# Optimization experiments

Measured on AMD Instinct MI355X. Metric: run time of the kernel, lower is better.

## Reference

```python
import jax, jax.numpy as jnp
import numpy as np

N_HEAD = 16
RMS_EPS = 1.1920928955078125e-07  # torch float32 finfo eps (F.rms_norm default)


def _apply_rotary(x, cos, sin):
    # x: [B,T,H,D], cos/sin: [1,T,1,D/2]
    d = x.shape[-1] // 2
    x1, x2 = x[..., :d], x[..., d:]
    return jnp.concatenate([x1 * cos + x2 * sin, -x1 * sin + x2 * cos], axis=-1)


def _rms_norm(x):
    var = jnp.mean(jnp.square(x), axis=-1, keepdims=True)
    return x * jax.lax.rsqrt(var + RMS_EPS)


def setup_inputs() -> dict:
    key = jax.random.key(0)
    ks = jax.random.split(key, 5)
    B, T, C, H = 2, 2048, 1024, N_HEAD
    D = C // H
    x = jax.random.normal(ks[0], (B, T, C), dtype=jnp.float32)
    cos = jax.random.uniform(ks[1], (1, T, 1, D // 2), dtype=jnp.float32)
    sin = jax.random.uniform(ks[2], (1, T, 1, D // 2), dtype=jnp.float32)
    kv_w = jax.random.normal(ks[3], (C, C), dtype=jnp.float32) * (C ** -0.5)
    proj_w = jax.random.normal(ks[4], (C, C), dtype=jnp.float32) * (C ** -0.5)
    return {"x": x, "cos": cos, "sin": sin, "kv_w": kv_w, "proj_w": proj_w, "window_left": 1024}


def reference(x, cos, sin, kv_w, proj_w, window_left):
    B, T, C = x.shape
    H = N_HEAD
    D = C // H
    scale = D ** -0.5

    q = x.reshape(B, T, H, D)                       # no Q projection
    kv = (x @ kv_w.T).reshape(B, T, H, D)           # tied K=V projection

    q = _rms_norm(_apply_rotary(q, cos, sin))
    kv = _rms_norm(_apply_rotary(kv, cos, sin))

    # scores: [B,H,T,T]
    scores = jnp.einsum('bqhd,bkhd->bhqk', q, kv) * scale

    pos = jnp.arange(T)
    dist = pos[:, None] - pos[None, :]              # query_pos - key_pos
    allowed = (dist >= 0) & (dist <= window_left)   # causal + sliding window
    scores = jnp.where(allowed[None, None], scores, -jnp.inf)

    attn = jax.nn.softmax(scores, axis=-1)
    out = jnp.einsum('bhqk,bkhd->bqhd', attn, kv).reshape(B, T, C)
    return out @ proj_w.T
```

## Files before the change

kernel.cpp:

```cpp
#include <hip/hip_runtime.h>
#include <hip/hip_bf16.h>

using u16 = unsigned short;
typedef __attribute__((ext_vector_type(8))) short short8v;
typedef __attribute__((ext_vector_type(4))) float f32x4;

#define MFMA16(a, b, c) __builtin_amdgcn_mfma_f32_16x16x32_bf16((a), (b), (c), 0, 0, 0)

#define GLOAD16(g, l) __builtin_amdgcn_global_load_lds(                       \
    (const __attribute__((address_space(1))) void*)(const void*)(g),          \
    (__attribute__((address_space(3))) void*)(void*)(l), 16, 0, 0)

static __device__ __forceinline__ u16 f2bf(float x) {
  __hip_bfloat16 h = __float2bfloat16(x);
  return __builtin_bit_cast(u16, h);
}

__global__ __launch_bounds__(256) void cast3_f32_bf16(const float* __restrict__ a, u16* __restrict__ da,
                                                      const float* __restrict__ b, u16* __restrict__ db,
                                                      const float* __restrict__ c, u16* __restrict__ dc) {
  int bid = blockIdx.x;
  const float* s; u16* d; int i;
  if (bid < 4096)      { s = a; d = da; i = bid; }
  else if (bid < 5120) { s = b; d = db; i = bid - 4096; }
  else                 { s = c; d = dc; i = bid - 5120; }
  int idx = (i * 256 + threadIdx.x) * 4;
  float4 v = *reinterpret_cast<const float4*>(s + idx);
  ushort4 o;
  o.x = f2bf(v.x); o.y = f2bf(v.y); o.z = f2bf(v.z); o.w = f2bf(v.w);
  *reinterpret_cast<ushort4*>(d + idx) = o;
}

__global__ __launch_bounds__(256) void gemm_bt(const u16* __restrict__ A,
                                               const u16* __restrict__ Bt,
                                               float* __restrict__ C,
                                               int M, int N, int K) {
  __shared__ u16 As[4][64 * 32];
  __shared__ u16 Bs[4][128 * 32];
  unsigned flat = blockIdx.y * gridDim.x + blockIdx.x;
  unsigned nwg = gridDim.x * gridDim.y;
  unsigned swz = (flat & 7) * (nwg >> 3) + (flat >> 3);
  int bm = swz % gridDim.x, bn = swz / gridDim.x;
  int tid = threadIdx.x;
  int wid = tid >> 6, l = tid & 63, lr = l & 15, lg = l >> 4;
  int wr = wid >> 1, wc = wid & 1;

  int srow = l >> 2, scol = (l & 3) * 8;
  const u16* Ag  = A  + (size_t)(bm * 64 + wid * 16 + srow) * K + scol;
  const u16* Bg0 = Bt + (size_t)(bn * 128 + wid * 32 + srow) * K + scol;
  const u16* Bg1 = Bg0 + (size_t)16 * K;

  f32x4 acc[2][4];
#pragma unroll
  for (int m = 0; m < 2; m++)
#pragma unroll
    for (int n = 0; n < 4; n++) acc[m][n] = (f32x4){0.f, 0.f, 0.f, 0.f};

  const int NT = K >> 5;

#pragma unroll
  for (int t = 0; t < 2; t++) {
    GLOAD16(Ag + t * 32, &As[t][wid * 512]);
    GLOAD16(Bg0 + t * 32, &Bs[t][wid * 1024]);
    GLOAD16(Bg1 + t * 32, &Bs[t][wid * 1024 + 512]);
  }

  for (int t = 0; t < NT; t++) {
    int cur = t & 3;
    if (t + 2 < NT) {
      int nb = (t + 2) & 3;
      int ko = (t + 2) * 32;
      GLOAD16(Ag + ko, &As[nb][wid * 512]);
      GLOAD16(Bg0 + ko, &Bs[nb][wid * 1024]);
      GLOAD16(Bg1 + ko, &Bs[nb][wid * 1024 + 512]);
    }
    if (t + 2 < NT)      asm volatile("s_waitcnt vmcnt(6)" ::: "memory");
    else if (t + 1 < NT) asm volatile("s_waitcnt vmcnt(3)" ::: "memory");
    else                 asm volatile("s_waitcnt vmcnt(0)" ::: "memory");
    __builtin_amdgcn_s_barrier();

    short8v af[2], bfr[4];
#pragma unroll
    for (int m = 0; m < 2; m++)
      af[m] = *reinterpret_cast<const short8v*>(&As[cur][(wr * 32 + m * 16 + lr) * 32 + lg * 8]);
#pragma unroll
    for (int n = 0; n < 4; n++)
      bfr[n] = *reinterpret_cast<const short8v*>(&Bs[cur][(wc * 64 + n * 16 + lr) * 32 + lg * 8]);
    asm volatile("s_waitcnt lgkmcnt(0)" ::: "memory");
    __builtin_amdgcn_sched_barrier(0);
    __builtin_amdgcn_s_setprio(1);
#pragma unroll
    for (int m = 0; m < 2; m++)
#pragma unroll
      for (int n = 0; n < 4; n++) acc[m][n] = MFMA16(af[m], bfr[n], acc[m][n]);
    __builtin_amdgcn_s_setprio(0);
  }

#pragma unroll
  for (int m = 0; m < 2; m++)
#pragma unroll
    for (int n = 0; n < 4; n++)
#pragma unroll
      for (int r = 0; r < 4; r++) {
        int row = bm * 64 + wr * 32 + m * 16 + lg * 4 + r;
        int col = bn * 128 + wc * 64 + n * 16 + lr;
        C[(size_t)row * N + col] = acc[m][n][r];
      }
}

__global__ __launch_bounds__(256) void rope_rms(const float* __restrict__ src,
                                                u16* __restrict__ dst,
                                                const float* __restrict__ cosp,
                                                const float* __restrict__ sinp,
                                                float scale) {
  int R = blockIdx.x * 4 + (threadIdx.x >> 6);
  int l = threadIdx.x & 63;
  int h = R & 15;
  int bt = R >> 4;
  int t = bt & 2047, b = bt >> 11;

  float v = src[((size_t)R << 6) + l];
  float p = __shfl_xor(v, 32);
  float c = cosp[(t << 5) + (l & 31)];
  float s = sinp[(t << 5) + (l & 31)];
  float r = v * c + ((l < 32) ? p * s : -p * s);
  float sq = r * r;
  sq += __shfl_xor(sq, 32);
  sq += __shfl_xor(sq, 16);
  sq += __shfl_xor(sq, 8);
  sq += __shfl_xor(sq, 4);
  sq += __shfl_xor(sq, 2);
  sq += __shfl_xor(sq, 1);
  float inv = rsqrtf(sq * (1.0f / 64.0f) + 1.1920928955078125e-07f) * scale;
  dst[((((size_t)b * 16 + h) * 2048 + t) << 6) + l] = f2bf(r * inv);
}

__global__ __launch_bounds__(256) void rope_rms_kv(const float* __restrict__ src,
                                                   u16* __restrict__ dst,
                                                   u16* __restrict__ dstT,
                                                   const float* __restrict__ cosp,
                                                   const float* __restrict__ sinp) {
  __shared__ u16 Ld[64][72];
  int t0 = blockIdx.x << 6;
  int bh = blockIdx.y;
  int b = bh >> 4, h = bh & 15;
  int tid = threadIdx.x;
  int w = tid >> 6, l = tid & 63;

  float cl, sl;
  for (int i = 0; i < 16; i++) {
    int tt = w * 16 + i;
    int t = t0 + tt;
    float v = src[((((size_t)b * 2048 + t) * 16 + h) << 6) + l];
    float p = __shfl_xor(v, 32);
    cl = cosp[(t << 5) + (l & 31)];
    sl = sinp[(t << 5) + (l & 31)];
    float r = v * cl + ((l < 32) ? p * sl : -p * sl);
    float sq = r * r;
    sq += __shfl_xor(sq, 32);
    sq += __shfl_xor(sq, 16);
    sq += __shfl_xor(sq, 8);
    sq += __shfl_xor(sq, 4);
    sq += __shfl_xor(sq, 2);
    sq += __shfl_xor(sq, 1);
    float inv = rsqrtf(sq * (1.0f / 64.0f) + 1.1920928955078125e-07f);
    u16 val = f2bf(r * inv);
    dst[(((size_t)bh * 2048 + t) << 6) + l] = val;
    Ld[tt][l] = val;
  }
  __syncthreads();
#pragma unroll
  for (int i = 0; i < 2; i++) {
    int c = tid + i * 256, dr = c >> 3, sg = c & 7;
    short8v v;
#pragma unroll
    for (int j = 0; j < 8; j++) v[j] = (short)Ld[sg * 8 + j][dr];
    *reinterpret_cast<short8v*>(dstT + ((size_t)bh * 64 + dr) * 2048 + t0 + sg * 8) = v;
  }
}

__global__ __launch_bounds__(256) void attn_swa(const u16* __restrict__ Q,
                                                const u16* __restrict__ KV,
                                                const u16* __restrict__ KVt,
                                                u16* __restrict__ O,
                                                const int* __restrict__ winp) {
  const int T = 2048;
  int bid = blockIdx.x;
  int bh = bid & 31;
  int qi = 31 - (bid >> 5);
  int q0 = qi << 6;
  int b = bh >> 4, h = bh & 15;
  int W = *winp;
  int tid = threadIdx.x;
  int wid = tid >> 6, l = tid & 63, lr = l & 15, lg = l >> 4;

  __shared__ u16 Kl[64][72];
  __shared__ u16 Vt[64][72];
  __shared__ u16 Pl[4][16][72];

  const u16* Qb = Q + (((size_t)bh * T + q0 + wid * 16 + lr) << 6);
  short8v aq0 = *reinterpret_cast<const short8v*>(Qb + lg * 8);
  short8v aq1 = *reinterpret_cast<const short8v*>(Qb + 32 + lg * 8);

  const short one_bf = (short)0x3F80;
  short8v vones = {one_bf, one_bf, one_bf, one_bf, one_bf, one_bf, one_bf, one_bf};

  float l_run[4];
  f32x4 oacc[4];
#pragma unroll
  for (int r = 0; r < 4; r++) l_run[r] = 0.f;
#pragma unroll
  for (int dt = 0; dt < 4; dt++) oacc[dt] = (f32x4){0.f, 0.f, 0.f, 0.f};

  int lo = q0 - W;
  if (lo < 0) lo = 0;
  lo &= ~63;

  const u16* KVbh  = KV + (((size_t)bh * T) << 6);
  const u16* KVtbh = KVt + ((size_t)bh << 6) * T;
  int r8 = tid >> 3, sg = tid & 7;

  short8v vK0 = *reinterpret_cast<const short8v*>(KVbh + ((size_t)(lo + r8) << 6) + sg * 8);
  short8v vK1 = *reinterpret_cast<const short8v*>(KVbh + ((size_t)(lo + r8 + 32) << 6) + sg * 8);
  short8v vV0 = *reinterpret_cast<const short8v*>(KVtbh + (size_t)r8 * T + lo + sg * 8);
  short8v vV1 = *reinterpret_cast<const short8v*>(KVtbh + (size_t)(r8 + 32) * T + lo + sg * 8);

  for (int kt = lo; kt <= q0; kt += 64) {
    __syncthreads();
    *reinterpret_cast<short8v*>(&Kl[r8][sg * 8]) = vK0;
    *reinterpret_cast<short8v*>(&Kl[r8 + 32][sg * 8]) = vK1;
    *reinterpret_cast<short8v*>(&Vt[r8][sg * 8]) = vV0;
    *reinterpret_cast<short8v*>(&Vt[r8 + 32][sg * 8]) = vV1;
    __syncthreads();
    if (kt < q0) {
      vK0 = *reinterpret_cast<const short8v*>(KVbh + ((size_t)(kt + 64 + r8) << 6) + sg * 8);
      vK1 = *reinterpret_cast<const short8v*>(KVbh + ((size_t)(kt + 64 + r8 + 32) << 6) + sg * 8);
      vV0 = *reinterpret_cast<const short8v*>(KVtbh + (size_t)r8 * T + kt + 64 + sg * 8);
      vV1 = *reinterpret_cast<const short8v*>(KVtbh + (size_t)(r8 + 32) * T + kt + 64 + sg * 8);
    }

    f32x4 s[4];
#pragma unroll
    for (int nt = 0; nt < 4; nt++) {
      s[nt] = (f32x4){0.f, 0.f, 0.f, 0.f};
      short8v b0 = *reinterpret_cast<const short8v*>(&Kl[nt * 16 + lr][lg * 8]);
      s[nt] = MFMA16(aq0, b0, s[nt]);
      short8v b1 = *reinterpret_cast<const short8v*>(&Kl[nt * 16 + lr][32 + lg * 8]);
      s[nt] = MFMA16(aq1, b1, s[nt]);
    }

    bool edge = (kt + 63 > q0 + wid * 16) || ((q0 - kt) + wid * 16 + 15 > W);
#pragma unroll
    for (int r = 0; r < 4; r++) {
      if (edge) {
        int t = q0 + wid * 16 + lg * 4 + r;
#pragma unroll
        for (int nt = 0; nt < 4; nt++) {
          int k = kt + nt * 16 + lr;
          float val = ((k <= t) && (t - k <= W)) ? s[nt][r] : -1e30f;
          Pl[wid][lg * 4 + r][nt * 16 + lr] = f2bf(exp2f(val - 12.f));
        }
      } else {
#pragma unroll
        for (int nt = 0; nt < 4; nt++)
          Pl[wid][lg * 4 + r][nt * 16 + lr] = f2bf(exp2f(s[nt][r] - 12.f));
      }
    }

    short8v ap0 = *reinterpret_cast<const short8v*>(&Pl[wid][lr][lg * 8]);
    short8v ap1 = *reinterpret_cast<const short8v*>(&Pl[wid][lr][32 + lg * 8]);
    f32x4 psum = (f32x4){0.f, 0.f, 0.f, 0.f};
    psum = MFMA16(ap0, vones, psum);
    psum = MFMA16(ap1, vones, psum);
#pragma unroll
    for (int dt = 0; dt < 4; dt++) {
      short8v v0 = *reinterpret_cast<const short8v*>(&Vt[dt * 16 + lr][lg * 8]);
      oacc[dt] = MFMA16(ap0, v0, oacc[dt]);
      short8v v1 = *reinterpret_cast<const short8v*>(&Vt[dt * 16 + lr][32 + lg * 8]);
      oacc[dt] = MFMA16(ap1, v1, oacc[dt]);
    }
#pragma unroll
    for (int r = 0; r < 4; r++) l_run[r] += psum[r];
  }

#pragma unroll
  for (int r = 0; r < 4; r++) {
    int t = q0 + wid * 16 + lg * 4 + r;
    float inv = 1.f / l_run[r];
#pragma unroll
    for (int dt = 0; dt < 4; dt++) {
      O[(((size_t)b * T + t) << 10) + (h << 6) + dt * 16 + lr] = f2bf(oacc[dt][r] * inv);
    }
  }
}

extern "C" void kernel_launch(void* const* d_in, const int* in_sizes, int n_in,
                              void* d_out, int out_size, void* d_ws, size_t ws_size,
                              hipStream_t stream) {
  (void)in_sizes; (void)n_in; (void)out_size; (void)ws_size;
  const float* x    = (const float*)d_in[0];
  const float* cosp = (const float*)d_in[1];
  const float* sinp = (const float*)d_in[2];
  const float* kvw  = (const float*)d_in[3];
  const float* pw   = (const float*)d_in[4];
  const int*   win  = (const int*)d_in[5];

  char* w = (char*)d_ws;
  u16*   xbf   = (u16*)(w);
  u16*   kvwbf = (u16*)(w + (8u << 20));
  u16*   pwbf  = (u16*)(w + (10u << 20));
  float* kvf   = (float*)(w + (12u << 20));
  u16*   kvt   = (u16*)(w + (12u << 20));
  u16*   aout  = (u16*)(w + (20u << 20));
  u16*   kvbf  = (u16*)(w + (28u << 20));
  u16*   qbf   = xbf;
  kvt = (u16*)(w + (36u << 20));

  cast3_f32_bf16<<<6144, 256, 0, stream>>>(x, xbf, kvw, kvwbf, pw, pwbf);

  gemm_bt<<<dim3(64, 8), 256, 0, stream>>>(xbf, kvwbf, kvf, 4096, 1024, 1024);

  rope_rms<<<16384, 256, 0, stream>>>(x, qbf, cosp, sinp, 0.18033688011112042f);
  rope_rms_kv<<<dim3(32, 32), 256, 0, stream>>>(kvf, kvbf, kvt, cosp, sinp);

  attn_swa<<<1024, 256, 0, stream>>>(qbf, kvbf, kvt, aout, win);

  gemm_bt<<<dim3(64, 8), 256, 0, stream>>>(aout, pwbf, (float*)d_out, 4096, 1024, 1024);
}
```

Measured before the change: 180.8 us.

## Split-K both GEMMs into two halves and fuse x cast into rope kernel

After: 192.5 us. 1.06x slower.

```diff
diff --git a/kernel.cpp b/kernel.cpp
--- a/kernel.cpp
+++ b/kernel.cpp
@@ -16,14 +16,12 @@
   return __builtin_bit_cast(u16, h);
 }
 
-__global__ __launch_bounds__(256) void cast3_f32_bf16(const float* __restrict__ a, u16* __restrict__ da,
-                                                      const float* __restrict__ b, u16* __restrict__ db,
-                                                      const float* __restrict__ c, u16* __restrict__ dc) {
+__global__ __launch_bounds__(256) void cast2_f32_bf16(const float* __restrict__ a, u16* __restrict__ da,
+                                                      const float* __restrict__ b, u16* __restrict__ db) {
   int bid = blockIdx.x;
   const float* s; u16* d; int i;
-  if (bid < 4096)      { s = a; d = da; i = bid; }
-  else if (bid < 5120) { s = b; d = db; i = bid - 4096; }
-  else                 { s = c; d = dc; i = bid - 5120; }
+  if (bid < 1024) { s = a; d = da; i = bid; }
+  else            { s = b; d = db; i = bid - 1024; }
   int idx = (i * 256 + threadIdx.x) * 4;
   float4 v = *reinterpret_cast<const float4*>(s + idx);
   ushort4 o;
@@ -31,24 +29,36 @@
   *reinterpret_cast<ushort4*>(d + idx) = o;
 }
 
+__global__ __launch_bounds__(256) void reduce2(const float* __restrict__ p0,
+                                               const float* __restrict__ p1,
+                                               float* __restrict__ out) {
+  int i = (blockIdx.x * 256 + threadIdx.x) * 4;
+  float4 a = *reinterpret_cast<const float4*>(p0 + i);
+  float4 b = *reinterpret_cast<const float4*>(p1 + i);
+  float4 o = {a.x + b.x, a.y + b.y, a.z + b.z, a.w + b.w};
+  *reinterpret_cast<float4*>(out + i) = o;
+}
+
 __global__ __launch_bounds__(256) void gemm_bt(const u16* __restrict__ A,
                                                const u16* __restrict__ Bt,
                                                float* __restrict__ C,
-                                               int M, int N, int K) {
+                                               int M, int N, int K, int K2) {
   __shared__ u16 As[4][64 * 32];
   __shared__ u16 Bs[4][128 * 32];
   unsigned flat = blockIdx.y * gridDim.x + blockIdx.x;
   unsigned nwg = gridDim.x * gridDim.y;
   unsigned swz = (flat & 7) * (nwg >> 3) + (flat >> 3);
   int bm = swz % gridDim.x, bn = swz / gridDim.x;
+  int z = blockIdx.z;
   int tid = threadIdx.x;
   int wid = tid >> 6, l = tid & 63, lr = l & 15, lg = l >> 4;
   int wr = wid >> 1, wc = wid & 1;
 
   int srow = l >> 2, scol = (l & 3) * 8;
-  const u16* Ag  = A  + (size_t)(bm * 64 + wid * 16 + srow) * K + scol;
-  const u16* Bg0 = Bt + (size_t)(bn * 128 + wid * 32 + srow) * K + scol;
+  const u16* Ag  = A  + (size_t)(bm * 64 + wid * 16 + srow) * K + z * K2 + scol;
+  const u16* Bg0 = Bt + (size_t)(bn * 128 + wid * 32 + srow) * K + z * K2 + scol;
   const u16* Bg1 = Bg0 + (size_t)16 * K;
+  C += (size_t)z * M * N;
 
   f32x4 acc[2][4];
 #pragma unroll
@@ -56,7 +66,7 @@
 #pragma unroll
     for (int n = 0; n < 4; n++) acc[m][n] = (f32x4){0.f, 0.f, 0.f, 0.f};
 
-  const int NT = K >> 5;
+  const int NT = K2 >> 5;
 
 #pragma unroll
   for (int t = 0; t < 2; t++) {
@@ -108,11 +118,12 @@
       }
 }
 
-__global__ __launch_bounds__(256) void rope_rms(const float* __restrict__ src,
-                                                u16* __restrict__ dst,
-                                                const float* __restrict__ cosp,
-                                                const float* __restrict__ sinp,
-                                                float scale) {
+__global__ __launch_bounds__(256) void rope_rms_x(const float* __restrict__ src,
+                                                  u16* __restrict__ xbf,
+                                                  u16* __restrict__ qdst,
+                                                  const float* __restrict__ cosp,
+                                                  const float* __restrict__ sinp,
+                                                  float scale) {
   int R = blockIdx.x * 4 + (threadIdx.x >> 6);
   int l = threadIdx.x & 63;
   int h = R & 15;
@@ -120,6 +131,7 @@
   int t = bt & 2047, b = bt >> 11;
 
   float v = src[((size_t)R << 6) + l];
+  xbf[((size_t)R << 6) + l] = f2bf(v);
   float p = __shfl_xor(v, 32);
   float c = cosp[(t << 5) + (l & 31)];
   float s = sinp[(t << 5) + (l & 31)];
@@ -132,10 +144,11 @@
   sq += __shfl_xor(sq, 2);
   sq += __shfl_xor(sq, 1);
   float inv = rsqrtf(sq * (1.0f / 64.0f) + 1.1920928955078125e-07f) * scale;
-  dst[((((size_t)b * 16 + h) * 2048 + t) << 6) + l] = f2bf(r * inv);
-}
-
-__global__ __launch_bounds__(256) void rope_rms_kv(const float* __restrict__ src,
+  qdst[((((size_t)b * 16 + h) * 2048 + t) << 6) + l] = f2bf(r * inv);
+}
+
+__global__ __launch_bounds__(256) void rope_rms_kv(const float* __restrict__ srcP0,
+                                                   const float* __restrict__ srcP1,
                                                    u16* __restrict__ dst,
                                                    u16* __restrict__ dstT,
                                                    const float* __restrict__ cosp,
@@ -147,14 +160,14 @@
   int tid = threadIdx.x;
   int w = tid >> 6, l = tid & 63;
 
-  float cl, sl;
   for (int i = 0; i < 16; i++) {
     int tt = w * 16 + i;
     int t = t0 + tt;
-    float v = src[((((size_t)b * 2048 + t) * 16 + h) << 6) + l];
+    size_t idx = ((((size_t)b * 2048 + t) * 16 + h) << 6) + l;
+    float v = srcP0[idx] + srcP1[idx];
     float p = __shfl_xor(v, 32);
-    cl = cosp[(t << 5) + (l & 31)];
-    sl = sinp[(t << 5) + (l & 31)];
+    float cl = cosp[(t << 5) + (l & 31)];
+    float sl = sinp[(t << 5) + (l & 31)];
     float r = v * cl + ((l < 32) ? p * sl : -p * sl);
     float sq = r * r;
     sq += __shfl_xor(sq, 32);
@@ -309,21 +322,24 @@
   u16*   xbf   = (u16*)(w);
   u16*   kvwbf = (u16*)(w + (8u << 20));
   u16*   pwbf  = (u16*)(w + (10u << 20));
-  float* kvf   = (float*)(w + (12u << 20));
-  u16*   kvt   = (u16*)(w + (12u << 20));
-  u16*   aout  = (u16*)(w + (20u << 20));
-  u16*   kvbf  = (u16*)(w + (28u << 20));
-  u16*   qbf   = xbf;
-  kvt = (u16*)(w + (36u << 20));
-
-  cast3_f32_bf16<<<6144, 256, 0, stream>>>(x, xbf, kvw, kvwbf, pw, pwbf);
-
-  gemm_bt<<<dim3(64, 8), 256, 0, stream>>>(xbf, kvwbf, kvf, 4096, 1024, 1024);
-
-  rope_rms<<<16384, 256, 0, stream>>>(x, qbf, cosp, sinp, 0.18033688011112042f);
-  rope_rms_kv<<<dim3(32, 32), 256, 0, stream>>>(kvf, kvbf, kvt, cosp, sinp);
+  float* kvfp  = (float*)(w + (12u << 20));
+  float* outp  = (float*)(w + (12u << 20));
+  u16*   kvbf  = (u16*)(w + (44u << 20));
+  u16*   kvt   = (u16*)(w + (52u << 20));
+  u16*   qbf   = (u16*)(w + (60u << 20));
+  u16*   aout  = (u16*)(w + (68u << 20));
+  const size_t PART = (size_t)4096 * 1024;
+
+  cast2_f32_bf16<<<2048, 256, 0, stream>>>(kvw, kvwbf, pw, pwbf);
+
+  rope_rms_x<<<16384, 256, 0, stream>>>(x, xbf, qbf, cosp, sinp, 0.18033688011112042f);
+
+  gemm_bt<<<dim3(64, 8, 2), 256, 0, stream>>>(xbf, kvwbf, kvfp, 4096, 1024, 1024, 512);
+
+  rope_rms_kv<<<dim3(32, 32), 256, 0, stream>>>(kvfp, kvfp + PART, kvbf, kvt, cosp, sinp);
 
   attn_swa<<<1024, 256, 0, stream>>>(qbf, kvbf, kvt, aout, win);
 
-  gemm_bt<<<dim3(64, 8), 256, 0, stream>>>(aout, pwbf, (float*)d_out, 4096, 1024, 1024);
-}
+  gemm_bt<<<dim3(64, 8, 2), 256, 0, stream>>>(aout, pwbf, outp, 4096, 1024, 1024, 512);
+  reduce2<<<4096, 256, 0, stream>>>(outp, outp + PART, (float*)d_out);
+}
```
